# Kernel tuning notes

Hardware: AMD Instinct MI355X
Metric: run time of the kernel (lower is better)

## Reference

```python
import jax, jax.numpy as jnp
import numpy as np

N = 100000   # nodes
E = 1600000  # edges
F = 128      # input node features
H = 128      # hidden_dim (conv2 out = H//2)
B = 50       # graphs in batch
C = 10       # fault classes


def _glorot(key, shape):
    fan_in, fan_out = shape
    lim = jnp.sqrt(6.0 / (fan_in + fan_out)).astype(jnp.float32)
    return jax.random.uniform(key, shape, jnp.float32, -lim, lim)


def setup_inputs() -> dict:
    key = jax.random.key(0)
    ks = jax.random.split(key, 8)
    x = jax.random.normal(ks[0], (N, F), jnp.float32)
    edge_index = jax.random.randint(ks[1], (2, E), 0, N, jnp.int32)
    batch = jnp.sort(jax.random.randint(ks[2], (N,), 0, B, jnp.int32))
    return {
        "x": x,
        "edge_index": edge_index,
        "batch": batch,
        "W1": _glorot(ks[3], (F, H)),
        "b1": jnp.zeros((H,), jnp.float32),
        "W2": _glorot(ks[4], (H, H // 2)),
        "b2": jnp.zeros((H // 2,), jnp.float32),
        "Wfc": _glorot(ks[5], (H // 2, C)),
        "bfc": jnp.zeros((C,), jnp.float32),
    }


def gcn_conv(h_in, W, b, src, dst, num_nodes):
    """PyG GCNConv with add_self_loops=True, edge_weight=None (all ones).
    out_i = sum_{j->i} (d_i^-1/2 d_j^-1/2) (W^T x_j) + d_i^-1 (W^T x_i) + b,
    where d includes the self-loop (+1). Self-loop handled analytically to
    avoid concatenating N extra edges."""
    h = h_in @ W                                                   # [N, out]
    ones_e = jnp.ones((src.shape[0],), h.dtype)
    deg = 1.0 + jax.ops.segment_sum(ones_e, dst, num_segments=num_nodes)
    dinv = jax.lax.rsqrt(deg)                                      # deg >= 1
    norm = dinv[src] * dinv[dst]                                   # [E]
    msgs = h[src] * norm[:, None]                                  # [E, out] gather
    agg = jax.ops.segment_sum(msgs, dst, num_segments=num_nodes)   # scatter-add
    return agg + h * (1.0 / deg)[:, None] + b


def reference(x, edge_index, batch, W1, b1, W2, b2, Wfc, bfc):
    src, dst = edge_index[0], edge_index[1]
    h = jax.nn.relu(gcn_conv(x, W1, b1, src, dst, N))
    # dropout(0.3) is identity in eval mode
    h = jax.nn.relu(gcn_conv(h, W2, b2, src, dst, N))
    # global mean pool over graphs
    sums = jax.ops.segment_sum(h, batch, num_segments=B)           # [B, H//2]
    counts = jax.ops.segment_sum(jnp.ones((N,), h.dtype), batch, num_segments=B)
    pooled = sums / jnp.maximum(counts, 1.0)[:, None]
    return pooled @ Wfc + bfc                                      # [B, C]
```

## Files before the change

kernel.cpp:

```cpp
#include <hip/hip_runtime.h>


#define IDX (blockIdx.x * (int)blockDim.x + (int)threadIdx.x)

__global__ void count_deg(const int* __restrict__ dst, int* __restrict__ cnt, int E) {
    int e = IDX;
    if (e < E) atomicAdd(&cnt[dst[e]], 1);
}

__global__ void compute_dinv(const int* __restrict__ cnt, float* __restrict__ dinv,
                             float* __restrict__ winv, int n) {
    int i = IDX;
    if (i < n) {
        float d = 1.0f + (float)cnt[i];
        dinv[i] = 1.0f / sqrtf(d);
        winv[i] = 1.0f / d;
    }
}

__global__ void scan1(const int* __restrict__ cnt, int* __restrict__ rs,
                      int* __restrict__ bsum, int n) {
    __shared__ int lds[256];
    int t = threadIdx.x;
    int base = blockIdx.x * 1024 + t * 4;
    int c0 = 0, c1 = 0, c2 = 0, c3 = 0;
    if (base + 3 < n) {
        int4 v = *(const int4*)&cnt[base];
        c0 = v.x; c1 = v.y; c2 = v.z; c3 = v.w;
    } else {
        if (base     < n) c0 = cnt[base];
        if (base + 1 < n) c1 = cnt[base + 1];
        if (base + 2 < n) c2 = cnt[base + 2];
        if (base + 3 < n) c3 = cnt[base + 3];
    }
    int s = c0 + c1 + c2 + c3;
    lds[t] = s; __syncthreads();
    for (int off = 1; off < 256; off <<= 1) {
        int v = (t >= off) ? lds[t - off] : 0;
        __syncthreads();
        lds[t] += v;
        __syncthreads();
    }
    int incl = lds[t];
    int excl = incl - s;
    if (t == 255) bsum[blockIdx.x] = incl;
    if (base     < n) rs[base]     = excl;
    if (base + 1 < n) rs[base + 1] = excl + c0;
    if (base + 2 < n) rs[base + 2] = excl + c0 + c1;
    if (base + 3 < n) rs[base + 3] = excl + c0 + c1 + c2;
}

__global__ void scan2(int* __restrict__ bsum, int nb) {
    __shared__ int lds[128];
    int t = threadIdx.x;
    int v = (t < nb) ? bsum[t] : 0;
    lds[t] = v; __syncthreads();
    for (int off = 1; off < 128; off <<= 1) {
        int u = (t >= off) ? lds[t - off] : 0;
        __syncthreads();
        lds[t] += u;
        __syncthreads();
    }
    if (t < nb) bsum[t] = lds[t] - v;
}

__global__ void scan3(int* __restrict__ rs, const int* __restrict__ bsum, int n, int E) {
    int i = IDX;
    if (i < n) rs[i] += bsum[i >> 10];
    if (i == 0) rs[n] = E;
}

__global__ void fill_csr(const int* __restrict__ src, const int* __restrict__ dst,
                         const int* __restrict__ rs, int* __restrict__ cursor,
                         const float* __restrict__ dinv,
                         int* __restrict__ csr_src, float* __restrict__ csr_w, int E) {
    int e = IDX;
    if (e < E) {
        int d = dst[e], s = src[e];
        int p = rs[d] + atomicAdd(&cursor[d], 1);
        csr_src[p] = s;
        csr_w[p]   = dinv[s] * dinv[d];
    }
}

__global__ __launch_bounds__(256) void gemm_k128(const float* __restrict__ X,
        const float* __restrict__ W, float* __restrict__ Y, int nrows, int outw) {
    __shared__ float ws[128][64];
    __shared__ float xs[64][128];
    const int t = threadIdx.x;
    const int row0 = blockIdx.x * 64;
    const int c0 = blockIdx.y * 64;

    #pragma unroll
    for (int i = 0; i < 8; ++i) {
        int idx = i * 256 + t;
        int k = idx >> 4, cq = idx & 15;
        float4 v = *(const float4*)&W[(size_t)k * outw + c0 + cq * 4];
        *(float4*)&ws[k][cq * 4] = v;
    }
    #pragma unroll
    for (int i = 0; i < 8; ++i) {
        int idx = i * 256 + t;
        int r = idx >> 5, kq = idx & 31;
        float4 v = make_float4(0.f, 0.f, 0.f, 0.f);
        if (row0 + r < nrows) v = *(const float4*)&X[(size_t)(row0 + r) * 128 + kq * 4];
        *(float4*)&xs[r][kq * 4] = v;
    }
    __syncthreads();

    const int r0  = (t >> 4) * 4;
    const int cc0 = (t & 15) * 4;
    float acc[4][4] = {};
    #pragma unroll 2
    for (int k0 = 0; k0 < 128; k0 += 4) {
        float xv[4][4], wv[4][4];
        #pragma unroll
        for (int i = 0; i < 4; ++i)
            *(float4*)xv[i] = *(const float4*)&xs[r0 + i][k0];
        #pragma unroll
        for (int kk = 0; kk < 4; ++kk)
            *(float4*)wv[kk] = *(const float4*)&ws[k0 + kk][cc0];
        #pragma unroll
        for (int i = 0; i < 4; ++i)
            #pragma unroll
            for (int kk = 0; kk < 4; ++kk)
                #pragma unroll
                for (int j = 0; j < 4; ++j)
                    acc[i][j] = fmaf(xv[i][kk], wv[kk][j], acc[i][j]);
    }
    #pragma unroll
    for (int i = 0; i < 4; ++i) {
        int row = row0 + r0 + i;
        if (row < nrows)
            *(float4*)&Y[(size_t)row * outw + c0 + cc0] = *(const float4*)acc[i];
    }
}

template<int FW, bool POOL>
__global__ __launch_bounds__(256) void aggregate(
        const float* __restrict__ h, const int* __restrict__ rs,
        const int* __restrict__ csr_src, const float* __restrict__ csr_w,
        const float* __restrict__ winv, const float* __restrict__ bias,
        const int* __restrict__ batch, float* __restrict__ pooled,
        float* __restrict__ out, int n) {
    int node = blockIdx.x * 4 + ((int)threadIdx.x >> 6);
    int lane = (int)threadIdx.x & 63;
    if (node >= n) return;
    int b0 = rs[node], b1 = rs[node + 1];

    float a0 = 0.f, a1 = 0.f;
    int e = b0;
    for (; e + 4 <= b1; e += 4) {
        int s0 = csr_src[e], s1 = csr_src[e+1], s2 = csr_src[e+2], s3 = csr_src[e+3];
        float w0 = csr_w[e], w1 = csr_w[e+1], w2 = csr_w[e+2], w3 = csr_w[e+3];
        if (FW == 128) {
            float2 v0 = *(const float2*)&h[(size_t)s0*128 + lane*2];
            float2 v1 = *(const float2*)&h[(size_t)s1*128 + lane*2];
            float2 v2 = *(const float2*)&h[(size_t)s2*128 + lane*2];
            float2 v3 = *(const float2*)&h[(size_t)s3*128 + lane*2];
            a0 += v0.x*w0 + v1.x*w1 + v2.x*w2 + v3.x*w3;
            a1 += v0.y*w0 + v1.y*w1 + v2.y*w2 + v3.y*w3;
        } else {
            float v0 = h[(size_t)s0*64 + lane];
            float v1 = h[(size_t)s1*64 + lane];
            float v2 = h[(size_t)s2*64 + lane];
            float v3 = h[(size_t)s3*64 + lane];
            a0 += v0*w0 + v1*w1 + v2*w2 + v3*w3;
        }
    }
    for (; e < b1; ++e) {
        int s = csr_src[e];
        float w = csr_w[e];
        if (FW == 128) {
            float2 v = *(const float2*)&h[(size_t)s*128 + lane*2];
            a0 += v.x * w; a1 += v.y * w;
        } else {
            a0 += h[(size_t)s*64 + lane] * w;
        }
    }

    float wself = winv[node];
    if (FW == 128) {
        float2 hv = *(const float2*)&h[(size_t)node*128 + lane*2];
        float2 bv = *(const float2*)&bias[lane*2];
        float o0 = fmaxf(a0 + hv.x * wself + bv.x, 0.f);
        float o1 = fmaxf(a1 + hv.y * wself + bv.y, 0.f);
        *(float2*)&out[(size_t)node*128 + lane*2] = make_float2(o0, o1);
    } else {
        float hv = h[(size_t)node*64 + lane];
        float o = fmaxf(a0 + hv * wself + bias[lane], 0.f);
        out[(size_t)node*64 + lane] = o;
        if (POOL) atomicAdd(&pooled[(size_t)batch[node]*64 + lane], o);
    }
}

__global__ void graph_counts(const int* __restrict__ batch, int* __restrict__ cntB,
                             int n, int B) {
    int b = (int)threadIdx.x;
    if (b < B) {
        int lo = 0, hi = n;
        while (lo < hi) { int mid = (lo + hi) >> 1; if (batch[mid] < b) lo = mid + 1; else hi = mid; }
        int start = lo;
        lo = 0; hi = n;
        while (lo < hi) { int mid = (lo + hi) >> 1; if (batch[mid] <= b) lo = mid + 1; else hi = mid; }
        cntB[b] = lo - start;
    }
}

__global__ void fc_kernel(const float* __restrict__ pooled, const int* __restrict__ cntB,
                          const float* __restrict__ Wfc, const float* __restrict__ bfc,
                          float* __restrict__ out) {
    int t = IDX;
    if (t < 50 * 10) {
        int b = t / 10, c = t % 10;
        float inv = 1.0f / fmaxf((float)cntB[b], 1.0f);
        float s = bfc[c];
        #pragma unroll
        for (int f = 0; f < 64; ++f)
            s = fmaf(pooled[b*64 + f] * inv, Wfc[f*10 + c], s);
        out[t] = s;
    }
}

extern "C" void kernel_launch(void* const* d_in, const int* in_sizes, int n_in,
                              void* d_out, int out_size, void* d_ws, size_t ws_size,
                              hipStream_t stream) {
    const float* x     = (const float*)d_in[0];
    const int*   ei    = (const int*)d_in[1];
    const int*   batch = (const int*)d_in[2];
    const float* W1    = (const float*)d_in[3];
    const float* b1    = (const float*)d_in[4];
    const float* W2    = (const float*)d_in[5];
    const float* b2    = (const float*)d_in[6];
    const float* Wfc   = (const float*)d_in[7];
    const float* bfc   = (const float*)d_in[8];
    float* out = (float*)d_out;

    const int n = in_sizes[2];
    const int E = in_sizes[1] / 2;
    const int* src = ei;
    const int* dst = ei + E;

    char* p = (char*)d_ws;
    auto alloc = [&](size_t bytes) { char* r = p; p += (bytes + 255) & ~(size_t)255; return r; };
    int*   cnt     = (int*)  alloc((size_t)n * 4);
    int*   cursor  = (int*)  alloc((size_t)n * 4);
    float* pooled  = (float*)alloc(50 * 64 * 4);
    size_t zbytes  = (size_t)(p - (char*)d_ws);
    int*   cntB    = (int*)  alloc(50 * 4);
    int*   bsum    = (int*)  alloc(128 * 4);
    int*   rs      = (int*)  alloc((size_t)(n + 1) * 4);
    int*   csr_src = (int*)  alloc((size_t)E * 4);
    float* csr_w   = (float*)alloc((size_t)E * 4);
    float* dinv    = (float*)alloc((size_t)n * 4);
    float* winv    = (float*)alloc((size_t)n * 4);
    float* h_raw   = (float*)alloc((size_t)n * 128 * 4);
    float* h_act   = (float*)alloc((size_t)n * 128 * 4);

    hipMemsetAsync(d_ws, 0, zbytes, stream);

    int eb    = (E + 255) / 256;
    int nb256 = (n + 255) / 256;
    int nscan = (n + 1023) / 1024;

    count_deg<<<eb, 256, 0, stream>>>(dst, cnt, E);
    compute_dinv<<<nb256, 256, 0, stream>>>(cnt, dinv, winv, n);
    scan1<<<nscan, 256, 0, stream>>>(cnt, rs, bsum, n);
    scan2<<<1, 128, 0, stream>>>(bsum, nscan);
    scan3<<<nb256, 256, 0, stream>>>(rs, bsum, n, E);
    fill_csr<<<eb, 256, 0, stream>>>(src, dst, rs, cursor, dinv, csr_src, csr_w, E);

    dim3 g1((n + 63) / 64, 2);
    gemm_k128<<<g1, 256, 0, stream>>>(x, W1, h_raw, n, 128);
    int nagg = (n + 3) / 4;
    aggregate<128, false><<<nagg, 256, 0, stream>>>(h_raw, rs, csr_src, csr_w,
                                                    winv, b1, batch, pooled, h_act, n);

    dim3 g2((n + 63) / 64, 1);
    gemm_k128<<<g2, 256, 0, stream>>>(h_act, W2, h_raw, n, 64);
    graph_counts<<<1, 64, 0, stream>>>(batch, cntB, n, 50);
    aggregate<64, true><<<nagg, 256, 0, stream>>>(h_raw, rs, csr_src, csr_w,
                                                  winv, b2, batch, pooled, h_act, n);

    fc_kernel<<<1, 512, 0, stream>>>(pooled, cntB, Wfc, bfc, out);
}
```

Baseline: 704.3 us.

## Pack CSR src/weight pairs and split wavefront into edge groups with float4 gathers

Stores each CSR entry's source index and normalization weight as one int2, so a single 8-byte load fetches both. The aggregation kernel splits each wavefront into 2 (FW=128) or 4 (FW=64) lane groups. Each group processes a strided subset of a node's edges with float4 row gathers, and the partial sums are combined with cross-lane shuffles. This aims to put more independent memory requests in flight per node and widen the gathers. The cost is extra shuffle work, and only one lane group writes the output and does the pooling atomics.

New measurement: 1.189 ms. 68.8% more time.

```diff
diff --git a/kernel.cpp b/kernel.cpp
--- a/kernel.cpp
+++ b/kernel.cpp
@@ -73,13 +73,12 @@
 __global__ void fill_csr(const int* __restrict__ src, const int* __restrict__ dst,
                          const int* __restrict__ rs, int* __restrict__ cursor,
                          const float* __restrict__ dinv,
-                         int* __restrict__ csr_src, float* __restrict__ csr_w, int E) {
+                         int2* __restrict__ csr_pk, int E) {
     int e = IDX;
     if (e < E) {
         int d = dst[e], s = src[e];
         int p = rs[d] + atomicAdd(&cursor[d], 1);
-        csr_src[p] = s;
-        csr_w[p]   = dinv[s] * dinv[d];
+        csr_pk[p] = make_int2(s, __float_as_int(dinv[s] * dinv[d]));
     }
 }
 
@@ -139,58 +138,87 @@
 template<int FW, bool POOL>
 __global__ __launch_bounds__(256) void aggregate(
         const float* __restrict__ h, const int* __restrict__ rs,
-        const int* __restrict__ csr_src, const float* __restrict__ csr_w,
+        const int2* __restrict__ csr_pk,
         const float* __restrict__ winv, const float* __restrict__ bias,
         const int* __restrict__ batch, float* __restrict__ pooled,
         float* __restrict__ out, int n) {
     int node = blockIdx.x * 4 + ((int)threadIdx.x >> 6);
     int lane = (int)threadIdx.x & 63;
     if (node >= n) return;
-    int b0 = rs[node], b1 = rs[node + 1];
-
-    float a0 = 0.f, a1 = 0.f;
-    int e = b0;
-    for (; e + 4 <= b1; e += 4) {
-        int s0 = csr_src[e], s1 = csr_src[e+1], s2 = csr_src[e+2], s3 = csr_src[e+3];
-        float w0 = csr_w[e], w1 = csr_w[e+1], w2 = csr_w[e+2], w3 = csr_w[e+3];
-        if (FW == 128) {
-            float2 v0 = *(const float2*)&h[(size_t)s0*128 + lane*2];
-            float2 v1 = *(const float2*)&h[(size_t)s1*128 + lane*2];
-            float2 v2 = *(const float2*)&h[(size_t)s2*128 + lane*2];
-            float2 v3 = *(const float2*)&h[(size_t)s3*128 + lane*2];
-            a0 += v0.x*w0 + v1.x*w1 + v2.x*w2 + v3.x*w3;
-            a1 += v0.y*w0 + v1.y*w1 + v2.y*w2 + v3.y*w3;
-        } else {
-            float v0 = h[(size_t)s0*64 + lane];
-            float v1 = h[(size_t)s1*64 + lane];
-            float v2 = h[(size_t)s2*64 + lane];
-            float v3 = h[(size_t)s3*64 + lane];
-            a0 += v0*w0 + v1*w1 + v2*w2 + v3*w3;
-        }
-    }
-    for (; e < b1; ++e) {
-        int s = csr_src[e];
-        float w = csr_w[e];
-        if (FW == 128) {
-            float2 v = *(const float2*)&h[(size_t)s*128 + lane*2];
-            a0 += v.x * w; a1 += v.y * w;
-        } else {
-            a0 += h[(size_t)s*64 + lane] * w;
-        }
-    }
-
-    float wself = winv[node];
+    const int b0 = rs[node], b1 = rs[node + 1];
+
+    constexpr int NG   = (FW == 128) ? 2 : 4;
+    const int grp = lane / (64 / NG);
+    const int fl  = lane % (64 / NG);
+
+    float4 acc = make_float4(0.f, 0.f, 0.f, 0.f);
+    int e = b0 + grp;
+
     if (FW == 128) {
-        float2 hv = *(const float2*)&h[(size_t)node*128 + lane*2];
-        float2 bv = *(const float2*)&bias[lane*2];
-        float o0 = fmaxf(a0 + hv.x * wself + bv.x, 0.f);
-        float o1 = fmaxf(a1 + hv.y * wself + bv.y, 0.f);
-        *(float2*)&out[(size_t)node*128 + lane*2] = make_float2(o0, o1);
+        for (; e + 6 < b1; e += 8) {
+            int2 p0 = csr_pk[e],     p1 = csr_pk[e + 2];
+            int2 p2 = csr_pk[e + 4], p3 = csr_pk[e + 6];
+            float4 v0 = *(const float4*)&h[(size_t)p0.x * 128 + fl * 4];
+            float4 v1 = *(const float4*)&h[(size_t)p1.x * 128 + fl * 4];
+            float4 v2 = *(const float4*)&h[(size_t)p2.x * 128 + fl * 4];
+            float4 v3 = *(const float4*)&h[(size_t)p3.x * 128 + fl * 4];
+            float w0 = __int_as_float(p0.y), w1 = __int_as_float(p1.y);
+            float w2 = __int_as_float(p2.y), w3 = __int_as_float(p3.y);
+            acc.x = fmaf(v0.x, w0, fmaf(v1.x, w1, fmaf(v2.x, w2, fmaf(v3.x, w3, acc.x))));
+            acc.y = fmaf(v0.y, w0, fmaf(v1.y, w1, fmaf(v2.y, w2, fmaf(v3.y, w3, acc.y))));
+            acc.z = fmaf(v0.z, w0, fmaf(v1.z, w1, fmaf(v2.z, w2, fmaf(v3.z, w3, acc.z))));
+            acc.w = fmaf(v0.w, w0, fmaf(v1.w, w1, fmaf(v2.w, w2, fmaf(v3.w, w3, acc.w))));
+        }
+        for (; e < b1; e += 2) {
+            int2 p = csr_pk[e];
+            float4 v = *(const float4*)&h[(size_t)p.x * 128 + fl * 4];
+            float w = __int_as_float(p.y);
+            acc.x = fmaf(v.x, w, acc.x); acc.y = fmaf(v.y, w, acc.y);
+            acc.z = fmaf(v.z, w, acc.z); acc.w = fmaf(v.w, w, acc.w);
+        }
     } else {
-        float hv = h[(size_t)node*64 + lane];
-        float o = fmaxf(a0 + hv * wself + bias[lane], 0.f);
-        out[(size_t)node*64 + lane] = o;
-        if (POOL) atomicAdd(&pooled[(size_t)batch[node]*64 + lane], o);
+        for (; e + 4 < b1; e += 8) {
+            int2 p0 = csr_pk[e], p1 = csr_pk[e + 4];
+            float4 v0 = *(const float4*)&h[(size_t)p0.x * 64 + fl * 4];
+            float4 v1 = *(const float4*)&h[(size_t)p1.x * 64 + fl * 4];
+            float w0 = __int_as_float(p0.y), w1 = __int_as_float(p1.y);
+            acc.x = fmaf(v0.x, w0, fmaf(v1.x, w1, acc.x));
+            acc.y = fmaf(v0.y, w0, fmaf(v1.y, w1, acc.y));
+            acc.z = fmaf(v0.z, w0, fmaf(v1.z, w1, acc.z));
+            acc.w = fmaf(v0.w, w0, fmaf(v1.w, w1, acc.w));
+        }
+        for (; e < b1; e += 4) {
+            int2 p = csr_pk[e];
+            float4 v = *(const float4*)&h[(size_t)p.x * 64 + fl * 4];
+            float w = __int_as_float(p.y);
+            acc.x = fmaf(v.x, w, acc.x); acc.y = fmaf(v.y, w, acc.y);
+            acc.z = fmaf(v.z, w, acc.z); acc.w = fmaf(v.w, w, acc.w);
+        }
+    }
+
+    if (FW == 64) {
+        acc.x += __shfl_xor(acc.x, 16); acc.y += __shfl_xor(acc.y, 16);
+        acc.z += __shfl_xor(acc.z, 16); acc.w += __shfl_xor(acc.w, 16);
+    }
+    acc.x += __shfl_xor(acc.x, 32); acc.y += __shfl_xor(acc.y, 32);
+    acc.z += __shfl_xor(acc.z, 32); acc.w += __shfl_xor(acc.w, 32);
+
+    const float wself = winv[node];
+    float4 hv = *(const float4*)&h[(size_t)node * FW + fl * 4];
+    float4 bv = *(const float4*)&bias[fl * 4];
+    float4 o;
+    o.x = fmaxf(fmaf(hv.x, wself, acc.x) + bv.x, 0.f);
+    o.y = fmaxf(fmaf(hv.y, wself, acc.y) + bv.y, 0.f);
+    o.z = fmaxf(fmaf(hv.z, wself, acc.z) + bv.z, 0.f);
+    o.w = fmaxf(fmaf(hv.w, wself, acc.w) + bv.w, 0.f);
+
+    if (grp == 0) {
+        *(float4*)&out[(size_t)node * FW + fl * 4] = o;
+        if (POOL) {
+            float* pb = &pooled[(size_t)batch[node] * 64 + fl * 4];
+            atomicAdd(pb + 0, o.x); atomicAdd(pb + 1, o.y);
+            atomicAdd(pb + 2, o.z); atomicAdd(pb + 3, o.w);
+        }
     }
 }
 
@@ -250,8 +278,7 @@
     int*   cntB    = (int*)  alloc(50 * 4);
     int*   bsum    = (int*)  alloc(128 * 4);
     int*   rs      = (int*)  alloc((size_t)(n + 1) * 4);
-    int*   csr_src = (int*)  alloc((size_t)E * 4);
-    float* csr_w   = (float*)alloc((size_t)E * 4);
+    int2*  csr_pk  = (int2*) alloc((size_t)E * 8);
     float* dinv    = (float*)alloc((size_t)n * 4);
     float* winv    = (float*)alloc((size_t)n * 4);
     float* h_raw   = (float*)alloc((size_t)n * 128 * 4);
@@ -268,18 +295,18 @@
     scan1<<<nscan, 256, 0, stream>>>(cnt, rs, bsum, n);
     scan2<<<1, 128, 0, stream>>>(bsum, nscan);
     scan3<<<nb256, 256, 0, stream>>>(rs, bsum, n, E);
-    fill_csr<<<eb, 256, 0, stream>>>(src, dst, rs, cursor, dinv, csr_src, csr_w, E);
+    fill_csr<<<eb, 256, 0, stream>>>(src, dst, rs, cursor, dinv, csr_pk, E);
 
     dim3 g1((n + 63) / 64, 2);
     gemm_k128<<<g1, 256, 0, stream>>>(x, W1, h_raw, n, 128);
     int nagg = (n + 3) / 4;
-    aggregate<128, false><<<nagg, 256, 0, stream>>>(h_raw, rs, csr_src, csr_w,
+    aggregate<128, false><<<nagg, 256, 0, stream>>>(h_raw, rs, csr_pk,
                                                     winv, b1, batch, pooled, h_act, n);
 
     dim3 g2((n + 63) / 64, 1);
     gemm_k128<<<g2, 256, 0, stream>>>(h_act, W2, h_raw, n, 64);
     graph_counts<<<1, 64, 0, stream>>>(batch, cntB, n, 50);
-    aggregate<64, true><<<nagg, 256, 0, stream>>>(h_raw, rs, csr_src, csr_w,
+    aggregate<64, true><<<nagg, 256, 0, stream>>>(h_raw, rs, csr_pk,
                                                   winv, b2, batch, pooled, h_act, n);
 
     fc_kernel<<<1, 512, 0, stream>>>(pooled, cntB, Wfc, bfc, out);
```

## Pack CSR source and weight into int2 and unroll aggregation by eight

Applied to the files above, without the earlier changes.

Interleaves each CSR edge's source index and normalization weight into one int2 array, so fill_csr makes one 8-byte store and aggregate makes one 8-byte load per edge instead of two separate arrays. The aggregation inner loop is unrolled from 4 to 8 edges with pairwise summation to keep more independent gathers in flight. The self-loop term now uses an fmaf. The scattered fill_csr stores become wider, and the tail loop handles more leftover edges because average degree is about 16.

Result: faster. 665.0 us (-5.6%).

```diff
diff --git a/kernel.cpp b/kernel.cpp
--- a/kernel.cpp
+++ b/kernel.cpp
@@ -73,13 +73,12 @@
 __global__ void fill_csr(const int* __restrict__ src, const int* __restrict__ dst,
                          const int* __restrict__ rs, int* __restrict__ cursor,
                          const float* __restrict__ dinv,
-                         int* __restrict__ csr_src, float* __restrict__ csr_w, int E) {
+                         int2* __restrict__ csr_pk, int E) {
     int e = IDX;
     if (e < E) {
         int d = dst[e], s = src[e];
         int p = rs[d] + atomicAdd(&cursor[d], 1);
-        csr_src[p] = s;
-        csr_w[p]   = dinv[s] * dinv[d];
+        csr_pk[p] = make_int2(s, __float_as_int(dinv[s] * dinv[d]));
     }
 }
 
@@ -139,43 +138,58 @@
 template<int FW, bool POOL>
 __global__ __launch_bounds__(256) void aggregate(
         const float* __restrict__ h, const int* __restrict__ rs,
-        const int* __restrict__ csr_src, const float* __restrict__ csr_w,
+        const int2* __restrict__ csr_pk,
         const float* __restrict__ winv, const float* __restrict__ bias,
         const int* __restrict__ batch, float* __restrict__ pooled,
         float* __restrict__ out, int n) {
     int node = blockIdx.x * 4 + ((int)threadIdx.x >> 6);
     int lane = (int)threadIdx.x & 63;
     if (node >= n) return;
-    int b0 = rs[node], b1 = rs[node + 1];
+    const int b0 = rs[node], b1 = rs[node + 1];
 
     float a0 = 0.f, a1 = 0.f;
     int e = b0;
-    for (; e + 4 <= b1; e += 4) {
-        int s0 = csr_src[e], s1 = csr_src[e+1], s2 = csr_src[e+2], s3 = csr_src[e+3];
-        float w0 = csr_w[e], w1 = csr_w[e+1], w2 = csr_w[e+2], w3 = csr_w[e+3];
+    for (; e + 8 <= b1; e += 8) {
+        int2 p0 = csr_pk[e],   p1 = csr_pk[e+1], p2 = csr_pk[e+2], p3 = csr_pk[e+3];
+        int2 p4 = csr_pk[e+4], p5 = csr_pk[e+5], p6 = csr_pk[e+6], p7 = csr_pk[e+7];
+        float w0 = __int_as_float(p0.y), w1 = __int_as_float(p1.y);
+        float w2 = __int_as_float(p2.y), w3 = __int_as_float(p3.y);
+        float w4 = __int_as_float(p4.y), w5 = __int_as_float(p5.y);
+        float w6 = __int_as_float(p6.y), w7 = __int_as_float(p7.y);
         if (FW == 128) {
-            float2 v0 = *(const float2*)&h[(size_t)s0*128 + lane*2];
-            float2 v1 = *(const float2*)&h[(size_t)s1*128 + lane*2];
-            float2 v2 = *(const float2*)&h[(size_t)s2*128 + lane*2];
-            float2 v3 = *(const float2*)&h[(size_t)s3*128 + lane*2];
-            a0 += v0.x*w0 + v1.x*w1 + v2.x*w2 + v3.x*w3;
-            a1 += v0.y*w0 + v1.y*w1 + v2.y*w2 + v3.y*w3;
+            float2 v0 = *(const float2*)&h[(size_t)p0.x*128 + lane*2];
+            float2 v1 = *(const float2*)&h[(size_t)p1.x*128 + lane*2];
+            float2 v2 = *(const float2*)&h[(size_t)p2.x*128 + lane*2];
+            float2 v3 = *(const float2*)&h[(size_t)p3.x*128 + lane*2];
+            float2 v4 = *(const float2*)&h[(size_t)p4.x*128 + lane*2];
+            float2 v5 = *(const float2*)&h[(size_t)p5.x*128 + lane*2];
+            float2 v6 = *(const float2*)&h[(size_t)p6.x*128 + lane*2];
+            float2 v7 = *(const float2*)&h[(size_t)p7.x*128 + lane*2];
+            a0 += (v0.x*w0 + v1.x*w1) + (v2.x*w2 + v3.x*w3)
+                + (v4.x*w4 + v5.x*w5) + (v6.x*w6 + v7.x*w7);
+            a1 += (v0.y*w0 + v1.y*w1) + (v2.y*w2 + v3.y*w3)
+                + (v4.y*w4 + v5.y*w5) + (v6.y*w6 + v7.y*w7);
         } else {
-            float v0 = h[(size_t)s0*64 + lane];
-            float v1 = h[(size_t)s1*64 + lane];
-            float v2 = h[(size_t)s2*64 + lane];
-            float v3 = h[(size_t)s3*64 + lane];
-            a0 += v0*w0 + v1*w1 + v2*w2 + v3*w3;
+            float v0 = h[(size_t)p0.x*64 + lane];
+            float v1 = h[(size_t)p1.x*64 + lane];
+            float v2 = h[(size_t)p2.x*64 + lane];
+            float v3 = h[(size_t)p3.x*64 + lane];
+            float v4 = h[(size_t)p4.x*64 + lane];
+            float v5 = h[(size_t)p5.x*64 + lane];
+            float v6 = h[(size_t)p6.x*64 + lane];
+            float v7 = h[(size_t)p7.x*64 + lane];
+            a0 += (v0*w0 + v1*w1) + (v2*w2 + v3*w3)
+                + (v4*w4 + v5*w5) + (v6*w6 + v7*w7);
         }
     }
     for (; e < b1; ++e) {
-        int s = csr_src[e];
-        float w = csr_w[e];
+        int2 p = csr_pk[e];
+        float w = __int_as_float(p.y);
         if (FW == 128) {
-            float2 v = *(const float2*)&h[(size_t)s*128 + lane*2];
+            float2 v = *(const float2*)&h[(size_t)p.x*128 + lane*2];
             a0 += v.x * w; a1 += v.y * w;
         } else {
-            a0 += h[(size_t)s*64 + lane] * w;
+            a0 += h[(size_t)p.x*64 + lane] * w;
         }
     }
 
@@ -183,12 +197,12 @@
     if (FW == 128) {
         float2 hv = *(const float2*)&h[(size_t)node*128 + lane*2];
         float2 bv = *(const float2*)&bias[lane*2];
-        float o0 = fmaxf(a0 + hv.x * wself + bv.x, 0.f);
-        float o1 = fmaxf(a1 + hv.y * wself + bv.y, 0.f);
+        float o0 = fmaxf(fmaf(hv.x, wself, a0) + bv.x, 0.f);
+        float o1 = fmaxf(fmaf(hv.y, wself, a1) + bv.y, 0.f);
         *(float2*)&out[(size_t)node*128 + lane*2] = make_float2(o0, o1);
     } else {
         float hv = h[(size_t)node*64 + lane];
-        float o = fmaxf(a0 + hv * wself + bias[lane], 0.f);
+        float o = fmaxf(fmaf(hv, wself, a0) + bias[lane], 0.f);
         out[(size_t)node*64 + lane] = o;
         if (POOL) atomicAdd(&pooled[(size_t)batch[node]*64 + lane], o);
     }
@@ -250,8 +264,7 @@
     int*   cntB    = (int*)  alloc(50 * 4);
     int*   bsum    = (int*)  alloc(128 * 4);
     int*   rs      = (int*)  alloc((size_t)(n + 1) * 4);
-    int*   csr_src = (int*)  alloc((size_t)E * 4);
-    float* csr_w   = (float*)alloc((size_t)E * 4);
+    int2*  csr_pk  = (int2*) alloc((size_t)E * 8);
     float* dinv    = (float*)alloc((size_t)n * 4);
     float* winv    = (float*)alloc((size_t)n * 4);
     float* h_raw   = (float*)alloc((size_t)n * 128 * 4);
@@ -268,18 +281,18 @@
     scan1<<<nscan, 256, 0, stream>>>(cnt, rs, bsum, n);
     scan2<<<1, 128, 0, stream>>>(bsum, nscan);
     scan3<<<nb256, 256, 0, stream>>>(rs, bsum, n, E);
-    fill_csr<<<eb, 256, 0, stream>>>(src, dst, rs, cursor, dinv, csr_src, csr_w, E);
+    fill_csr<<<eb, 256, 0, stream>>>(src, dst, rs, cursor, dinv, csr_pk, E);
 
     dim3 g1((n + 63) / 64, 2);
     gemm_k128<<<g1, 256, 0, stream>>>(x, W1, h_raw, n, 128);
     int nagg = (n + 3) / 4;
-    aggregate<128, false><<<nagg, 256, 0, stream>>>(h_raw, rs, csr_src, csr_w,
+    aggregate<128, false><<<nagg, 256, 0, stream>>>(h_raw, rs, csr_pk,
                                                     winv, b1, batch, pooled, h_act, n);
 
     dim3 g2((n + 63) / 64, 1);
     gemm_k128<<<g2, 256, 0, stream>>>(h_act, W2, h_raw, n, 64);
     graph_counts<<<1, 64, 0, stream>>>(batch, cntB, n, 50);
-    aggregate<64, true><<<nagg, 256, 0, stream>>>(h_raw, rs, csr_src, csr_w,
+    aggregate<64, true><<<nagg, 256, 0, stream>>>(h_raw, rs, csr_pk,
                                                   winv, b2, batch, pooled, h_act, n);
 
     fc_kernel<<<1, 512, 0, stream>>>(pooled, cntB, Wfc, bfc, out);
```

## Store pre-scaled GEMM outputs in bf16 and drop per-edge weights

Applied to the files above, without the earlier changes.

The GEMM epilogue now multiplies each row by dinv[row] and writes it as bf16. Aggregation then sums neighbor rows with no per-edge weight, adds the self row, and scales once by dinv[node]. This removes the csr_w array, the winv array and half the gather bytes, and the inner loop is unrolled to 8 edges. The second layer also stops writing its fp32 output because only the pool needs it. The cost is bf16 rounding of the hidden activations, which may loosen accuracy.

Measured after the change: 650.1 us. 1.08x faster.

```diff
diff --git a/kernel.cpp b/kernel.cpp
--- a/kernel.cpp
+++ b/kernel.cpp
@@ -2,20 +2,21 @@
 
 
 #define IDX (blockIdx.x * (int)blockDim.x + (int)threadIdx.x)
+
+__device__ __forceinline__ unsigned short f2bf(float f) {
+    union { float f; unsigned u; } c{f};
+    unsigned u = c.u;
+    return (unsigned short)((u + 0x7fffu + ((u >> 16) & 1u)) >> 16);
+}
 
 __global__ void count_deg(const int* __restrict__ dst, int* __restrict__ cnt, int E) {
     int e = IDX;
     if (e < E) atomicAdd(&cnt[dst[e]], 1);
 }
 
-__global__ void compute_dinv(const int* __restrict__ cnt, float* __restrict__ dinv,
-                             float* __restrict__ winv, int n) {
+__global__ void compute_dinv(const int* __restrict__ cnt, float* __restrict__ dinv, int n) {
     int i = IDX;
-    if (i < n) {
-        float d = 1.0f + (float)cnt[i];
-        dinv[i] = 1.0f / sqrtf(d);
-        winv[i] = 1.0f / d;
-    }
+    if (i < n) dinv[i] = 1.0f / sqrtf(1.0f + (float)cnt[i]);
 }
 
 __global__ void scan1(const int* __restrict__ cnt, int* __restrict__ rs,
@@ -72,19 +73,18 @@
 
 __global__ void fill_csr(const int* __restrict__ src, const int* __restrict__ dst,
                          const int* __restrict__ rs, int* __restrict__ cursor,
-                         const float* __restrict__ dinv,
-                         int* __restrict__ csr_src, float* __restrict__ csr_w, int E) {
+                         int* __restrict__ csr, int E) {
     int e = IDX;
     if (e < E) {
-        int d = dst[e], s = src[e];
+        int d = dst[e];
         int p = rs[d] + atomicAdd(&cursor[d], 1);
-        csr_src[p] = s;
-        csr_w[p]   = dinv[s] * dinv[d];
-    }
-}
-
-__global__ __launch_bounds__(256) void gemm_k128(const float* __restrict__ X,
-        const float* __restrict__ W, float* __restrict__ Y, int nrows, int outw) {
+        csr[p] = src[e];
+    }
+}
+
+__global__ __launch_bounds__(256) void gemm_k128_bf(const float* __restrict__ X,
+        const float* __restrict__ W, const float* __restrict__ dinv,
+        unsigned short* __restrict__ Ybf, int nrows, int outw) {
     __shared__ float ws[128][64];
     __shared__ float xs[64][128];
     const int t = threadIdx.x;
@@ -131,66 +131,85 @@
     #pragma unroll
     for (int i = 0; i < 4; ++i) {
         int row = row0 + r0 + i;
-        if (row < nrows)
-            *(float4*)&Y[(size_t)row * outw + c0 + cc0] = *(const float4*)acc[i];
+        if (row < nrows) {
+            float s = dinv[row];
+            ushort4 st;
+            st.x = f2bf(acc[i][0] * s); st.y = f2bf(acc[i][1] * s);
+            st.z = f2bf(acc[i][2] * s); st.w = f2bf(acc[i][3] * s);
+            *(ushort4*)&Ybf[(size_t)row * outw + c0 + cc0] = st;
+        }
     }
 }
 
 template<int FW, bool POOL>
-__global__ __launch_bounds__(256) void aggregate(
-        const float* __restrict__ h, const int* __restrict__ rs,
-        const int* __restrict__ csr_src, const float* __restrict__ csr_w,
-        const float* __restrict__ winv, const float* __restrict__ bias,
-        const int* __restrict__ batch, float* __restrict__ pooled,
-        float* __restrict__ out, int n) {
+__global__ __launch_bounds__(256) void aggregate_bf(
+        const unsigned short* __restrict__ hbf, const int* __restrict__ rs,
+        const int* __restrict__ csr, const float* __restrict__ dinv,
+        const float* __restrict__ bias, const int* __restrict__ batch,
+        float* __restrict__ pooled, float* __restrict__ out, int n) {
     int node = blockIdx.x * 4 + ((int)threadIdx.x >> 6);
     int lane = (int)threadIdx.x & 63;
     if (node >= n) return;
-    int b0 = rs[node], b1 = rs[node + 1];
+    const int b0 = rs[node], b1 = rs[node + 1];
 
     float a0 = 0.f, a1 = 0.f;
     int e = b0;
-    for (; e + 4 <= b1; e += 4) {
-        int s0 = csr_src[e], s1 = csr_src[e+1], s2 = csr_src[e+2], s3 = csr_src[e+3];
-        float w0 = csr_w[e], w1 = csr_w[e+1], w2 = csr_w[e+2], w3 = csr_w[e+3];
+    for (; e + 8 <= b1; e += 8) {
+        int s0 = csr[e],   s1 = csr[e+1], s2 = csr[e+2], s3 = csr[e+3];
+        int s4 = csr[e+4], s5 = csr[e+5], s6 = csr[e+6], s7 = csr[e+7];
         if (FW == 128) {
-            float2 v0 = *(const float2*)&h[(size_t)s0*128 + lane*2];
-            float2 v1 = *(const float2*)&h[(size_t)s1*128 + lane*2];
-            float2 v2 = *(const float2*)&h[(size_t)s2*128 + lane*2];
-            float2 v3 = *(const float2*)&h[(size_t)s3*128 + lane*2];
-            a0 += v0.x*w0 + v1.x*w1 + v2.x*w2 + v3.x*w3;
-            a1 += v0.y*w0 + v1.y*w1 + v2.y*w2 + v3.y*w3;
+            unsigned v0 = *(const unsigned*)&hbf[(size_t)s0*128 + lane*2];
+            unsigned v1 = *(const unsigned*)&hbf[(size_t)s1*128 + lane*2];
+            unsigned v2 = *(const unsigned*)&hbf[(size_t)s2*128 + lane*2];
+            unsigned v3 = *(const unsigned*)&hbf[(size_t)s3*128 + lane*2];
+            unsigned v4 = *(const unsigned*)&hbf[(size_t)s4*128 + lane*2];
+            unsigned v5 = *(const unsigned*)&hbf[(size_t)s5*128 + lane*2];
+            unsigned v6 = *(const unsigned*)&hbf[(size_t)s6*128 + lane*2];
+            unsigned v7 = *(const unsigned*)&hbf[(size_t)s7*128 + lane*2];
+            a0 += (__uint_as_float(v0 << 16) + __uint_as_float(v1 << 16))
+                + (__uint_as_float(v2 << 16) + __uint_as_float(v3 << 16))
+                + (__uint_as_float(v4 << 16) + __uint_as_float(v5 << 16))
+                + (__uint_as_float(v6 << 16) + __uint_as_float(v7 << 16));
+            a1 += (__uint_as_float(v0 & 0xffff0000u) + __uint_as_float(v1 & 0xffff0000u))
+                + (__uint_as_float(v2 & 0xffff0000u) + __uint_as_float(v3 & 0xffff0000u))
+                + (__uint_as_float(v4 & 0xffff0000u) + __uint_as_float(v5 & 0xffff0000u))
+                + (__uint_as_float(v6 & 0xffff0000u) + __uint_as_float(v7 & 0xffff0000u));
         } else {
-            float v0 = h[(size_t)s0*64 + lane];
-            float v1 = h[(size_t)s1*64 + lane];
-            float v2 = h[(size_t)s2*64 + lane];
-            float v3 = h[(size_t)s3*64 + lane];
-            a0 += v0*w0 + v1*w1 + v2*w2 + v3*w3;
+            unsigned u0 = hbf[(size_t)s0*64 + lane], u1 = hbf[(size_t)s1*64 + lane];
+            unsigned u2 = hbf[(size_t)s2*64 + lane], u3 = hbf[(size_t)s3*64 + lane];
+            unsigned u4 = hbf[(size_t)s4*64 + lane], u5 = hbf[(size_t)s5*64 + lane];
+            unsigned u6 = hbf[(size_t)s6*64 + lane], u7 = hbf[(size_t)s7*64 + lane];
+            a0 += (__uint_as_float(u0 << 16) + __uint_as_float(u1 << 16))
+                + (__uint_as_float(u2 << 16) + __uint_as_float(u3 << 16))
+                + (__uint_as_float(u4 << 16) + __uint_as_float(u5 << 16))
+                + (__uint_as_float(u6 << 16) + __uint_as_float(u7 << 16));
         }
     }
     for (; e < b1; ++e) {
-        int s = csr_src[e];
-        float w = csr_w[e];
+        int s = csr[e];
         if (FW == 128) {
-            float2 v = *(const float2*)&h[(size_t)s*128 + lane*2];
-            a0 += v.x * w; a1 += v.y * w;
+            unsigned v = *(const unsigned*)&hbf[(size_t)s*128 + lane*2];
+            a0 += __uint_as_float(v << 16);
+            a1 += __uint_as_float(v & 0xffff0000u);
         } else {
-            a0 += h[(size_t)s*64 + lane] * w;
+            a0 += __uint_as_float((unsigned)hbf[(size_t)s*64 + lane] << 16);
         }
     }
 
-    float wself = winv[node];
+    const float dn = dinv[node];
     if (FW == 128) {
-        float2 hv = *(const float2*)&h[(size_t)node*128 + lane*2];
+        unsigned vs = *(const unsigned*)&hbf[(size_t)node*128 + lane*2];
+        a0 += __uint_as_float(vs << 16);
+        a1 += __uint_as_float(vs & 0xffff0000u);
         float2 bv = *(const float2*)&bias[lane*2];
-        float o0 = fmaxf(a0 + hv.x * wself + bv.x, 0.f);
-        float o1 = fmaxf(a1 + hv.y * wself + bv.y, 0.f);
+        float o0 = fmaxf(fmaf(a0, dn, bv.x), 0.f);
+        float o1 = fmaxf(fmaf(a1, dn, bv.y), 0.f);
         *(float2*)&out[(size_t)node*128 + lane*2] = make_float2(o0, o1);
     } else {
-        float hv = h[(size_t)node*64 + lane];
-        float o = fmaxf(a0 + hv * wself + bias[lane], 0.f);
-        out[(size_t)node*64 + lane] = o;
+        a0 += __uint_as_float((unsigned)hbf[(size_t)node*64 + lane] << 16);
+        float o = fmaxf(fmaf(a0, dn, bias[lane]), 0.f);
         if (POOL) atomicAdd(&pooled[(size_t)batch[node]*64 + lane], o);
+        else out[(size_t)node*64 + lane] = o;
     }
 }
 
@@ -250,11 +269,10 @@
     int*   cntB    = (int*)  alloc(50 * 4);
     int*   bsum    = (int*)  alloc(128 * 4);
     int*   rs      = (int*)  alloc((size_t)(n + 1) * 4);
-    int*   csr_src = (int*)  alloc((size_t)E * 4);
-    float* csr_w   = (float*)alloc((size_t)E * 4);
+    int*   csr     = (int*)  alloc((size_t)E * 4);
     float* dinv    = (float*)alloc((size_t)n * 4);
-    float* winv    = (float*)alloc((size_t)n * 4);
-    float* h_raw   = (float*)alloc((size_t)n * 128 * 4);
+    unsigned short* hbf1 = (unsigned short*)alloc((size_t)n * 128 * 2);
+    unsigned short* hbf2 = (unsigned short*)alloc((size_t)n * 64 * 2);
     float* h_act   = (float*)alloc((size_t)n * 128 * 4);
 
     hipMemsetAsync(d_ws, 0, zbytes, stream);
@@ -264,23 +282,23 @@
     int nscan = (n + 1023) / 1024;
 
     count_deg<<<eb, 256, 0, stream>>>(dst, cnt, E);
-    compute_dinv<<<nb256, 256, 0, stream>>>(cnt, dinv, winv, n);
+    compute_dinv<<<nb256, 256, 0, stream>>>(cnt, dinv, n);
     scan1<<<nscan, 256, 0, stream>>>(cnt, rs, bsum, n);
     scan2<<<1, 128, 0, stream>>>(bsum, nscan);
     scan3<<<nb256, 256, 0, stream>>>(rs, bsum, n, E);
-    fill_csr<<<eb, 256, 0, stream>>>(src, dst, rs, cursor, dinv, csr_src, csr_w, E);
+    fill_csr<<<eb, 256, 0, stream>>>(src, dst, rs, cursor, csr, E);
 
     dim3 g1((n + 63) / 64, 2);
-    gemm_k128<<<g1, 256, 0, stream>>>(x, W1, h_raw, n, 128);
+    gemm_k128_bf<<<g1, 256, 0, stream>>>(x, W1, dinv, hbf1, n, 128);
     int nagg = (n + 3) / 4;
-    aggregate<128, false><<<nagg, 256, 0, stream>>>(h_raw, rs, csr_src, csr_w,
-                                                    winv, b1, batch, pooled, h_act, n);
+    aggregate_bf<128, false><<<nagg, 256, 0, stream>>>(hbf1, rs, csr, dinv,
+                                                       b1, batch, pooled, h_act, n);
 
     dim3 g2((n + 63) / 64, 1);
-    gemm_k128<<<g2, 256, 0, stream>>>(h_act, W2, h_raw, n, 64);
+    gemm_k128_bf<<<g2, 256, 0, stream>>>(h_act, W2, dinv, hbf2, n, 64);
     graph_counts<<<1, 64, 0, stream>>>(batch, cntB, n, 50);
-    aggregate<64, true><<<nagg, 256, 0, stream>>>(h_raw, rs, csr_src, csr_w,
-                                                  winv, b2, batch, pooled, h_act, n);
+    aggregate_bf<64, true><<<nagg, 256, 0, stream>>>(hbf2, rs, csr, dinv,
+                                                     b2, batch, pooled, nullptr, n);
 
     fc_kernel<<<1, 512, 0, stream>>>(pooled, cntB, Wfc, bfc, out);
 }
```
